# Optimization experiments

Measured on AMD Instinct MI355X. Metric: run time of the kernel, lower is better.

## Reference

```python
import jax, jax.numpy as jnp
import numpy as np

D_MODEL = 96
D_INNER = 192   # int(ssm_ratio * d_model)
D_STATE = 16
DT_RANK = 6    # ceil(96/16)
K_GROUP = 4
B, H, W = 2, 64, 64


def _selective_scan(xs, dts, A, Bs, Cs, Dskip, dt_bias):
    """Mamba selective scan.
    xs, dts: (B, K, Di, L); A: (K, Di, N); Bs, Cs: (B, K, N, L);
    Dskip, dt_bias: (K, Di). Returns y: (B, K, Di, L)."""
    delta = jax.nn.softplus(dts + dt_bias[None, :, :, None])     # (B,K,Di,L)
    u_t = jnp.moveaxis(xs, -1, 0)      # (L,B,K,Di)
    d_t = jnp.moveaxis(delta, -1, 0)   # (L,B,K,Di)
    b_t = jnp.moveaxis(Bs, -1, 0)      # (L,B,K,N)
    c_t = jnp.moveaxis(Cs, -1, 0)      # (L,B,K,N)

    def step(h, inp):
        u, dt, b, c = inp
        dA = jnp.exp(dt[..., None] * A)                          # (B,K,Di,N)
        h = h * dA + (dt * u)[..., None] * b[:, :, None, :]      # (B,K,Di,N)
        y = jnp.einsum('bkdn,bkn->bkd', h, c)
        return h, y

    h0 = jnp.zeros(xs.shape[:3] + (A.shape[-1],), xs.dtype)
    _, ys = jax.lax.scan(step, h0, (u_t, d_t, b_t, c_t))         # (L,B,K,Di)
    return jnp.moveaxis(ys, 0, -1) + Dskip[None, :, :, None] * xs


def setup_inputs() -> dict:
    key = jax.random.key(0)
    ks = jax.random.split(key, 10)
    x = jax.random.normal(ks[0], (B, H, W, D_MODEL), dtype=jnp.float32)
    in_proj_w = jax.random.normal(ks[1], (2 * D_INNER, D_MODEL), jnp.float32) * (D_MODEL ** -0.5)
    conv_w = jax.random.normal(ks[2], (D_INNER, 1, 3, 3), jnp.float32) * 0.1   # depthwise
    conv_b = jax.random.normal(ks[3], (D_INNER,), jnp.float32) * 0.01
    x_proj_weight = jax.random.normal(ks[4], (K_GROUP, DT_RANK + 2 * D_STATE, D_INNER), jnp.float32) * (D_INNER ** -0.5)
    dt_projs_weight = jax.random.uniform(ks[5], (K_GROUP, D_INNER, DT_RANK), jnp.float32,
                                         -(DT_RANK ** -0.5), DT_RANK ** -0.5)
    # bias ~ inv_softplus(dt) for dt in [0.001, 0.1]
    dt_projs_bias = jax.random.uniform(ks[6], (K_GROUP, D_INNER), jnp.float32, -6.5, -2.5)
    # S4D real init: A_log[d, n] = log(n+1)
    A_logs = jnp.log(jnp.tile(jnp.arange(1, D_STATE + 1, dtype=jnp.float32),
                              (K_GROUP * D_INNER, 1)))
    Ds = jnp.ones((K_GROUP * D_INNER,), jnp.float32)
    out_norm_w = jnp.ones((D_INNER,), jnp.float32)
    out_norm_b = jnp.zeros((D_INNER,), jnp.float32)
    out_proj_w = jax.random.normal(ks[7], (D_MODEL, D_INNER), jnp.float32) * (D_INNER ** -0.5)
    return dict(x=x, in_proj_w=in_proj_w, conv_w=conv_w, conv_b=conv_b,
                x_proj_weight=x_proj_weight, dt_projs_weight=dt_projs_weight,
                dt_projs_bias=dt_projs_bias, A_logs=A_logs, Ds=Ds,
                out_norm_w=out_norm_w, out_norm_b=out_norm_b, out_proj_w=out_proj_w)


def reference(x, in_proj_w, conv_w, conv_b, x_proj_weight, dt_projs_weight,
              dt_projs_bias, A_logs, Ds, out_norm_w, out_norm_b, out_proj_w):
    b, h, w, _ = x.shape
    xz = x @ in_proj_w.T                              # (B,H,W,2*Di)
    xp, z = jnp.split(xz, 2, axis=-1)
    xp = jnp.transpose(xp, (0, 3, 1, 2))              # (B,Di,H,W)
    xp = jax.lax.conv_general_dilated(
        xp, conv_w, (1, 1), 'SAME', feature_group_count=conv_w.shape[0],
        dimension_numbers=('NCHW', 'OIHW', 'NCHW')) + conv_b[None, :, None, None]
    xp = jax.nn.silu(xp)
    di = xp.shape[1]
    L = h * w
    # 4-way cross-scan: row-major, col-major, and their reverses
    x_hw = xp.reshape(b, di, L)
    x_wh = jnp.transpose(xp, (0, 1, 3, 2)).reshape(b, di, L)
    x_hwwh = jnp.stack([x_hw, x_wh], axis=1)          # (B,2,Di,L)
    xs = jnp.concatenate([x_hwwh, jnp.flip(x_hwwh, axis=-1)], axis=1)  # (B,4,Di,L)

    x_dbl = jnp.einsum('bkdl,kcd->bkcl', xs, x_proj_weight)
    R = dt_projs_weight.shape[-1]
    N = A_logs.shape[-1]
    dts_r = x_dbl[:, :, :R]
    Bs = x_dbl[:, :, R:R + N]                         # (B,K,N,L)
    Cs = x_dbl[:, :, R + N:]                          # (B,K,N,L)
    dts = jnp.einsum('bkrl,kdr->bkdl', dts_r, dt_projs_weight)
    A = -jnp.exp(A_logs).reshape(K_GROUP, di, N)
    Dskip = Ds.reshape(K_GROUP, di)

    out_y = _selective_scan(xs, dts, A, Bs, Cs, Dskip, dt_projs_bias)  # (B,4,Di,L)

    # un-scan: flip back the reversed dirs, un-transpose the wh dirs, sum
    inv_y = jnp.flip(out_y[:, 2:4], axis=-1)
    wh_y = jnp.transpose(out_y[:, 1].reshape(b, di, w, h), (0, 1, 3, 2)).reshape(b, di, L)
    invwh_y = jnp.transpose(inv_y[:, 1].reshape(b, di, w, h), (0, 1, 3, 2)).reshape(b, di, L)
    y = out_y[:, 0] + inv_y[:, 0] + wh_y + invwh_y    # (B,Di,L)

    y = jnp.transpose(y, (0, 2, 1))                   # (B,L,Di)
    mu = y.mean(-1, keepdims=True)
    var = ((y - mu) ** 2).mean(-1, keepdims=True)
    y = (y - mu) * jax.lax.rsqrt(var + 1e-5) * out_norm_w + out_norm_b
    y = y.reshape(b, h, w, di) + z                    # residual with gate branch (note: add, per source)
    out = y @ out_proj_w.T                            # (B,H,W,d_model)
    return jnp.transpose(out, (0, 3, 1, 2))           # (B,d_model,H,W)
```

## Files before the change

kernel.cpp:

```cpp
#include <hip/hip_runtime.h>
#include <math.h>

#define BB 2
#define HH 64
#define WW 64
#define LL 4096
#define CIN 96
#define DI 192
#define KG 4
#define NST 16
#define RNK 6
#define NCH 128
#define CHL 32

__device__ __forceinline__ int rowmap(int k, int p) {
  if (k == 0) return p;
  if (k == 1) return ((p & 63) << 6) | (p >> 6);
  if (k == 2) return (LL - 1) - p;
  int q = (LL - 1) - p;
  return ((q & 63) << 6) | (q >> 6);
}

__device__ __forceinline__ void powers(float r, float pw[NST]) {
  pw[0] = r;
  pw[1] = r * r;
  pw[2] = pw[1] * r;
  pw[3] = pw[1] * pw[1];
  pw[4] = pw[3] * r;
  pw[5] = pw[3] * pw[1];
  pw[6] = pw[3] * pw[2];
  pw[7] = pw[3] * pw[3];
  pw[8] = pw[7] * r;
  pw[9] = pw[7] * pw[1];
  pw[10] = pw[7] * pw[2];
  pw[11] = pw[7] * pw[3];
  pw[12] = pw[7] * pw[4];
  pw[13] = pw[7] * pw[5];
  pw[14] = pw[7] * pw[6];
  pw[15] = pw[7] * pw[7];
}

__device__ __forceinline__ void softplus_sig(float x, float& delta, float& r) {
  float e = __expf(fminf(x, 20.f));
  r = __builtin_amdgcn_rcpf(1.f + e);
  delta = (x > 20.f) ? x : -__logf(r);
}

__global__ __launch_bounds__(256) void k_inproj(const float* __restrict__ x,
    const float* __restrict__ w, float* __restrict__ xp_pre, float* __restrict__ z) {
  __shared__ float xt[64 * 97];
  __shared__ float wt[64 * 97];
  const int tile = blockIdx.x, og = blockIdx.y, t = threadIdx.x;
  const int tok0 = tile * 64;
  for (int idx = t; idx < 64 * 96; idx += 256) {
    int r = idx / 96, c = idx - r * 96;
    xt[r * 97 + c] = x[(tok0 + r) * 96 + c];
    wt[r * 97 + c] = w[(og * 64 + r) * 96 + c];
  }
  __syncthreads();
  const int tr = t >> 4, tc = t & 15;
  float acc[4][4];
#pragma unroll
  for (int i = 0; i < 4; ++i)
#pragma unroll
    for (int j = 0; j < 4; ++j) acc[i][j] = 0.f;
  for (int kk = 0; kk < 96; ++kk) {
    float a[4], bv[4];
#pragma unroll
    for (int i = 0; i < 4; ++i) a[i] = xt[(tr * 4 + i) * 97 + kk];
#pragma unroll
    for (int j = 0; j < 4; ++j) bv[j] = wt[(tc * 4 + j) * 97 + kk];
#pragma unroll
    for (int i = 0; i < 4; ++i)
#pragma unroll
      for (int j = 0; j < 4; ++j) acc[i][j] += a[i] * bv[j];
  }
#pragma unroll
  for (int i = 0; i < 4; ++i) {
    int tok = tok0 + tr * 4 + i;
    int b = tok >> 12, l = tok & 4095;
#pragma unroll
    for (int j = 0; j < 4; ++j) {
      int oc = og * 64 + tc * 4 + j;
      float v = acc[i][j];
      if (oc < DI) xp_pre[(b * DI + oc) * LL + l] = v;
      else         z[tok * DI + (oc - DI)] = v;
    }
  }
}

__global__ __launch_bounds__(256) void k_conv(const float* __restrict__ xp_pre,
    const float* __restrict__ cw, const float* __restrict__ cb,
    float* __restrict__ xpT, float* __restrict__ ycomb) {
  int idx = blockIdx.x * 256 + threadIdx.x;
  ycomb[idx] = 0.f;
  int l = idx & 4095;
  int bd = idx >> 12;
  int d = bd % DI, b = bd / DI;
  int h = l >> 6, wq = l & 63;
  const float* base = xp_pre + bd * LL;
  const float* wf = cw + d * 9;
  float acc = cb[d];
#pragma unroll
  for (int dh = -1; dh <= 1; ++dh) {
    int h2 = h + dh;
    if (h2 < 0 || h2 >= HH) continue;
#pragma unroll
    for (int dw = -1; dw <= 1; ++dw) {
      int w2 = wq + dw;
      if (w2 < 0 || w2 >= WW) continue;
      acc += base[h2 * WW + w2] * wf[(dh + 1) * 3 + (dw + 1)];
    }
  }
  float s = acc / (1.f + __expf(-acc));
  xpT[(b * LL + l) * DI + d] = s;
}

__global__ __launch_bounds__(256) void k_xdbl(const float* __restrict__ xpT,
    const float* __restrict__ xpw, float* __restrict__ xdT) {
  __shared__ float xs[32 * 196];
  __shared__ float wt[40 * 196];
  const int bk = blockIdx.x, tile = blockIdx.y, t = threadIdx.x;
  const int b = bk >> 2, k = bk & 3;
  for (int idx = t; idx < 32 * 192; idx += 256) {
    int r = idx / 192, c = idx - r * 192;
    xs[r * 196 + c] = xpT[(b * LL + rowmap(k, tile * 32 + r)) * DI + c];
  }
  for (int idx = t; idx < 40 * 192; idx += 256) {
    int r = idx / 192, c = idx - r * 192;
    wt[r * 196 + c] = (r < 38) ? xpw[k * 38 * 192 + idx] : 0.f;
  }
  __syncthreads();
  const int j = t >> 3;
  const int c0 = t & 7;
  float acc[5] = {0.f, 0.f, 0.f, 0.f, 0.f};
  const float4* xs4 = (const float4*)xs + j * 49;
  for (int d4 = 0; d4 < 48; ++d4) {
    float4 xv = xs4[d4];
#pragma unroll
    for (int jj = 0; jj < 5; ++jj) {
      const float4 wv = ((const float4*)wt)[(c0 + 8 * jj) * 49 + d4];
      acc[jj] += xv.x * wv.x + xv.y * wv.y + xv.z * wv.z + xv.w * wv.w;
    }
  }
  const int tok = bk * LL + tile * 32 + j;
#pragma unroll
  for (int jj = 0; jj < 5; ++jj) {
    int c = c0 + 8 * jj;
    if (c < 38) {
      int oc = (c < 6) ? 32 + c : c - 6;
      xdT[tok * 40 + oc] = acc[jj];
    }
  }
}

__global__ __launch_bounds__(192) void k_scanA(const float* __restrict__ xdT,
    const float* __restrict__ xpT, const float* __restrict__ dtw,
    const float* __restrict__ dtb, float* __restrict__ hfin, float* __restrict__ dsum) {
  const int d = threadIdx.x, bk = blockIdx.x, ch = blockIdx.y;
  const int b = bk >> 2, k = bk & 3;
  float w[RNK];
#pragma unroll
  for (int r = 0; r < RNK; ++r) w[r] = dtw[(k * DI + d) * RNK + r];
  const float bias = dtb[k * DI + d];
  float h[NST];
#pragma unroll
  for (int n = 0; n < NST; ++n) h[n] = 0.f;
  float ds = 0.f;
  const float* row = xdT + ((size_t)bk * LL + ch * CHL) * 40;
  const float* ubase = xpT + (size_t)b * LL * DI;
#pragma unroll 4
  for (int ll = 0; ll < CHL; ++ll) {
    int p = ch * CHL + ll;
    const float4* r4 = (const float4*)(row + ll * 40);
    float4 b0 = r4[0], b1 = r4[1], b2 = r4[2], b3 = r4[3];
    float4 dt4 = r4[8];
    float2 dt2 = ((const float2*)(row + ll * 40 + 36))[0];
    float xr = bias + dt4.x * w[0] + dt4.y * w[1] + dt4.z * w[2] + dt4.w * w[3]
             + dt2.x * w[4] + dt2.y * w[5];
    float delta, rdec;
    softplus_sig(xr, delta, rdec);
    float u = ubase[rowmap(k, p) * DI + d];
    float du = delta * u;
    ds += delta;
    float pw[NST];
    powers(rdec, pw);
    const float bn[NST] = {b0.x, b0.y, b0.z, b0.w, b1.x, b1.y, b1.z, b1.w,
                           b2.x, b2.y, b2.z, b2.w, b3.x, b3.y, b3.z, b3.w};
#pragma unroll
    for (int n = 0; n < NST; ++n) h[n] = h[n] * pw[n] + du * bn[n];
  }
  float4* hf = (float4*)(hfin + ((size_t)(bk * DI + d) * NCH + ch) * NST);
#pragma unroll
  for (int n = 0; n < 4; ++n)
    hf[n] = make_float4(h[4 * n], h[4 * n + 1], h[4 * n + 2], h[4 * n + 3]);
  dsum[(bk * DI + d) * NCH + ch] = ds;
}

__global__ __launch_bounds__(256) void k_scanB(const float* __restrict__ hfin,
    const float* __restrict__ dsum, const float* __restrict__ A_logs, float* __restrict__ hin) {
  int idx = blockIdx.x * 256 + threadIdx.x;
  int n = idx & 15, bkd = idx >> 4;
  int d = bkd % DI, k = (bkd / DI) & 3;
  float A = -__expf(A_logs[(k * DI + d) * NST + n]);
  float s = 0.f;
  for (int c = 0; c < NCH; ++c) {
    int o = (bkd * NCH + c) * NST + n;
    float f = hfin[o];
    hin[o] = s;
    s = s * __expf(A * dsum[bkd * NCH + c]) + f;
  }
}

__global__ __launch_bounds__(192) void k_scanC(const float* __restrict__ xdT,
    const float* __restrict__ xpT, const float* __restrict__ dtw,
    const float* __restrict__ dtb, const float* __restrict__ hin, float* __restrict__ ycomb) {
  const int d = threadIdx.x, bk = blockIdx.x, ch = blockIdx.y;
  const int b = bk >> 2, k = bk & 3;
  float w[RNK];
#pragma unroll
  for (int r = 0; r < RNK; ++r) w[r] = dtw[(k * DI + d) * RNK + r];
  const float bias = dtb[k * DI + d];
  float h[NST];
  const float4* hi = (const float4*)(hin + ((size_t)(bk * DI + d) * NCH + ch) * NST);
#pragma unroll
  for (int n = 0; n < 4; ++n) {
    float4 v = hi[n];
    h[4 * n] = v.x; h[4 * n + 1] = v.y; h[4 * n + 2] = v.z; h[4 * n + 3] = v.w;
  }
  const float* row = xdT + ((size_t)bk * LL + ch * CHL) * 40;
  const float* ubase = xpT + (size_t)b * LL * DI;
  float* yb = ycomb + (size_t)b * LL * DI;
#pragma unroll 4
  for (int ll = 0; ll < CHL; ++ll) {
    int p = ch * CHL + ll;
    const float4* r4 = (const float4*)(row + ll * 40);
    float4 b0 = r4[0], b1 = r4[1], b2 = r4[2], b3 = r4[3];
    float4 c0 = r4[4], c1 = r4[5], c2 = r4[6], c3 = r4[7];
    float4 dt4 = r4[8];
    float2 dt2 = ((const float2*)(row + ll * 40 + 36))[0];
    float xr = bias + dt4.x * w[0] + dt4.y * w[1] + dt4.z * w[2] + dt4.w * w[3]
             + dt2.x * w[4] + dt2.y * w[5];
    float delta, rdec;
    softplus_sig(xr, delta, rdec);
    int rr = rowmap(k, p);
    float u = ubase[rr * DI + d];
    float du = delta * u;
    float pw[NST];
    powers(rdec, pw);
    const float bn[NST] = {b0.x, b0.y, b0.z, b0.w, b1.x, b1.y, b1.z, b1.w,
                           b2.x, b2.y, b2.z, b2.w, b3.x, b3.y, b3.z, b3.w};
    const float cn[NST] = {c0.x, c0.y, c0.z, c0.w, c1.x, c1.y, c1.z, c1.w,
                           c2.x, c2.y, c2.z, c2.w, c3.x, c3.y, c3.z, c3.w};
    float y = 0.f;
#pragma unroll
    for (int n = 0; n < NST; ++n) {
      h[n] = h[n] * pw[n] + du * bn[n];
      y += h[n] * cn[n];
    }
    atomicAdd(&yb[rr * DI + d], y);
  }
}

__global__ __launch_bounds__(256) void k_norm(const float* __restrict__ ycomb,
    const float* __restrict__ xpT, const float* __restrict__ Ds, const float* __restrict__ z,
    const float* __restrict__ nw, const float* __restrict__ nb, float* __restrict__ yn) {
  int row = blockIdx.x * 4 + (threadIdx.x >> 6);
  int lane = threadIdx.x & 63;
  float v[3];
#pragma unroll
  for (int i = 0; i < 3; ++i) {
    int d = lane + i * 64;
    float dsv = Ds[d] + Ds[DI + d] + Ds[2 * DI + d] + Ds[3 * DI + d];
    v[i] = ycomb[row * DI + d] + dsv * xpT[row * DI + d];
  }
  float s1 = v[0] + v[1] + v[2];
  float s2 = v[0] * v[0] + v[1] * v[1] + v[2] * v[2];
#pragma unroll
  for (int off = 32; off >= 1; off >>= 1) {
    s1 += __shfl_xor(s1, off);
    s2 += __shfl_xor(s2, off);
  }
  float mu = s1 * (1.f / DI);
  float var = s2 * (1.f / DI) - mu * mu;
  float rstd = rsqrtf(var + 1e-5f);
#pragma unroll
  for (int i = 0; i < 3; ++i) {
    int d = lane + i * 64;
    yn[row * DI + d] = (v[i] - mu) * rstd * nw[d] + nb[d] + z[row * DI + d];
  }
}

__global__ __launch_bounds__(256) void k_outproj(const float* __restrict__ yn,
    const float* __restrict__ opw, float* __restrict__ out) {
  __shared__ float yt[32 * 193];
  __shared__ float wt[32 * 193];
  const int tile = blockIdx.x, og = blockIdx.y, t = threadIdx.x;
  const int tok0 = tile * 32;
  for (int idx = t; idx < 32 * 192; idx += 256) {
    int r = idx / 192, c = idx - r * 192;
    yt[r * 193 + c] = yn[(tok0 + r) * DI + c];
    wt[r * 193 + c] = opw[(og * 32 + r) * DI + c];
  }
  __syncthreads();
  const int tr = t >> 4, tc = t & 15;
  float acc[2][2] = {{0.f, 0.f}, {0.f, 0.f}};
  for (int dd = 0; dd < 192; ++dd) {
    float a0 = yt[(tr * 2) * 193 + dd], a1 = yt[(tr * 2 + 1) * 193 + dd];
    float b0 = wt[(tc * 2) * 193 + dd], b1 = wt[(tc * 2 + 1) * 193 + dd];
    acc[0][0] += a0 * b0; acc[0][1] += a0 * b1;
    acc[1][0] += a1 * b0; acc[1][1] += a1 * b1;
  }
#pragma unroll
  for (int i = 0; i < 2; ++i) {
    int tok = tok0 + tr * 2 + i;
    int b = tok >> 12, l = tok & 4095;
#pragma unroll
    for (int j = 0; j < 2; ++j) {
      int oc = og * 32 + tc * 2 + j;
      out[(b * CIN + oc) * LL + l] = acc[i][j];
    }
  }
}

extern "C" void kernel_launch(void* const* d_in, const int* in_sizes, int n_in,
                              void* d_out, int out_size, void* d_ws, size_t ws_size,
                              hipStream_t stream) {
  const float* x    = (const float*)d_in[0];
  const float* ipw  = (const float*)d_in[1];
  const float* cw   = (const float*)d_in[2];
  const float* cb   = (const float*)d_in[3];
  const float* xpw  = (const float*)d_in[4];
  const float* dtw  = (const float*)d_in[5];
  const float* dtb  = (const float*)d_in[6];
  const float* Alog = (const float*)d_in[7];
  const float* Ds   = (const float*)d_in[8];
  const float* nw   = (const float*)d_in[9];
  const float* nb   = (const float*)d_in[10];
  const float* opw  = (const float*)d_in[11];
  float* out = (float*)d_out;
  float* ws = (float*)d_ws;

  float* xp_pre = ws;
  float* xpT    = ws + 1572864;
  float* z      = ws + 3145728;
  float* xdT    = ws + 4718592;
  float* hfin   = ws + 6029312;
  float* hin    = ws + 9175040;
  float* dsum   = ws + 12320768;
  float* ycomb  = ws + 12517376;
  float* yn     = xp_pre;

  k_inproj<<<dim3(128, 6), 256, 0, stream>>>(x, ipw, xp_pre, z);
  k_conv<<<6144, 256, 0, stream>>>(xp_pre, cw, cb, xpT, ycomb);
  k_xdbl<<<dim3(8, 128), 256, 0, stream>>>(xpT, xpw, xdT);
  k_scanA<<<dim3(8, NCH), 192, 0, stream>>>(xdT, xpT, dtw, dtb, hfin, dsum);
  k_scanB<<<96, 256, 0, stream>>>(hfin, dsum, Alog, hin);
  k_scanC<<<dim3(8, NCH), 192, 0, stream>>>(xdT, xpT, dtw, dtb, hin, ycomb);
  k_norm<<<2048, 256, 0, stream>>>(ycomb, xpT, Ds, z, nw, nb, yn);
  k_outproj<<<dim3(256, 3), 256, 0, stream>>>(yn, opw, out);
}
```

Measured before the change: 230.8 us.

## Store x_dbl in spatial order, tile conv in shared memory, restructure x_proj

Result: slower. 301.4 us (+30.6%).

```diff
diff --git a/kernel.cpp b/kernel.cpp
--- a/kernel.cpp
+++ b/kernel.cpp
@@ -22,22 +22,12 @@
 }
 
 __device__ __forceinline__ void powers(float r, float pw[NST]) {
-  pw[0] = r;
-  pw[1] = r * r;
-  pw[2] = pw[1] * r;
-  pw[3] = pw[1] * pw[1];
-  pw[4] = pw[3] * r;
-  pw[5] = pw[3] * pw[1];
-  pw[6] = pw[3] * pw[2];
+  pw[0] = r;  pw[1] = r * r;  pw[2] = pw[1] * r;  pw[3] = pw[1] * pw[1];
+  pw[4] = pw[3] * r;  pw[5] = pw[3] * pw[1];  pw[6] = pw[3] * pw[2];
   pw[7] = pw[3] * pw[3];
-  pw[8] = pw[7] * r;
-  pw[9] = pw[7] * pw[1];
-  pw[10] = pw[7] * pw[2];
-  pw[11] = pw[7] * pw[3];
-  pw[12] = pw[7] * pw[4];
-  pw[13] = pw[7] * pw[5];
-  pw[14] = pw[7] * pw[6];
-  pw[15] = pw[7] * pw[7];
+  pw[8] = pw[7] * r;  pw[9] = pw[7] * pw[1];  pw[10] = pw[7] * pw[2];
+  pw[11] = pw[7] * pw[3];  pw[12] = pw[7] * pw[4];  pw[13] = pw[7] * pw[5];
+  pw[14] = pw[7] * pw[6];  pw[15] = pw[7] * pw[7];
 }
 
 __device__ __forceinline__ void softplus_sig(float x, float& delta, float& r) {
@@ -92,65 +82,92 @@
 __global__ __launch_bounds__(256) void k_conv(const float* __restrict__ xp_pre,
     const float* __restrict__ cw, const float* __restrict__ cb,
     float* __restrict__ xpT, float* __restrict__ ycomb) {
-  int idx = blockIdx.x * 256 + threadIdx.x;
-  ycomb[idx] = 0.f;
-  int l = idx & 4095;
-  int bd = idx >> 12;
-  int d = bd % DI, b = bd / DI;
-  int h = l >> 6, wq = l & 63;
-  const float* base = xp_pre + bd * LL;
-  const float* wf = cw + d * 9;
-  float acc = cb[d];
-#pragma unroll
-  for (int dh = -1; dh <= 1; ++dh) {
-    int h2 = h + dh;
-    if (h2 < 0 || h2 >= HH) continue;
-#pragma unroll
-    for (int dw = -1; dw <= 1; ++dw) {
-      int w2 = wq + dw;
-      if (w2 < 0 || w2 >= WW) continue;
-      acc += base[h2 * WW + w2] * wf[(dh + 1) * 3 + (dw + 1)];
-    }
-  }
-  float s = acc / (1.f + __expf(-acc));
-  xpT[(b * LL + l) * DI + d] = s;
+  __shared__ float ls[3 * 64 * 67];
+  const int t = threadIdx.x;
+  const int h = blockIdx.x;
+  const int b = blockIdx.y / 3, d0 = (blockIdx.y % 3) * 64;
+  int gid = (blockIdx.y * 64 + blockIdx.x) * 256 + t;
+#pragma unroll
+  for (int j = 0; j < 16; ++j) ycomb[gid + 98304 * j] = 0.f;
+  for (int i = t; i < 3 * 64; i += 256) {
+    ls[i * 67 + 0] = 0.f;
+    ls[i * 67 + 65] = 0.f;
+  }
+  for (int i = t; i < 3 * 64 * 64; i += 256) {
+    int rr = i >> 12, rem = i & 4095;
+    int dl = rem >> 6, w = rem & 63;
+    int h2 = h + rr - 1;
+    float v = (h2 >= 0 && h2 < HH)
+        ? xp_pre[((size_t)(b * DI + d0 + dl)) * LL + h2 * WW + w] : 0.f;
+    ls[(rr * 64 + dl) * 67 + w + 1] = v;
+  }
+  __syncthreads();
+  const int dl = t & 63, wg = t >> 6;
+  const int d = d0 + dl;
+  float wf[9];
+#pragma unroll
+  for (int j = 0; j < 9; ++j) wf[j] = cw[d * 9 + j];
+  const float bias = cb[d];
+#pragma unroll 4
+  for (int i = 0; i < 16; ++i) {
+    int w = wg + 4 * i;
+    float acc = bias;
+#pragma unroll
+    for (int rr = 0; rr < 3; ++rr)
+#pragma unroll
+      for (int dw = 0; dw < 3; ++dw)
+        acc += ls[(rr * 64 + dl) * 67 + w + dw] * wf[rr * 3 + dw];
+    float s = acc / (1.f + __expf(-acc));
+    xpT[((size_t)(b * LL + h * WW + w)) * DI + d] = s;
+  }
 }
 
 __global__ __launch_bounds__(256) void k_xdbl(const float* __restrict__ xpT,
     const float* __restrict__ xpw, float* __restrict__ xdT) {
-  __shared__ float xs[32 * 196];
-  __shared__ float wt[40 * 196];
-  const int bk = blockIdx.x, tile = blockIdx.y, t = threadIdx.x;
-  const int b = bk >> 2, k = bk & 3;
-  for (int idx = t; idx < 32 * 192; idx += 256) {
-    int r = idx / 192, c = idx - r * 192;
-    xs[r * 196 + c] = xpT[(b * LL + rowmap(k, tile * 32 + r)) * DI + c];
-  }
-  for (int idx = t; idx < 40 * 192; idx += 256) {
-    int r = idx / 192, c = idx - r * 192;
-    wt[r * 196 + c] = (r < 38) ? xpw[k * 38 * 192 + idx] : 0.f;
-  }
-  __syncthreads();
-  const int j = t >> 3;
-  const int c0 = t & 7;
-  float acc[5] = {0.f, 0.f, 0.f, 0.f, 0.f};
-  const float4* xs4 = (const float4*)xs + j * 49;
-  for (int d4 = 0; d4 < 48; ++d4) {
-    float4 xv = xs4[d4];
-#pragma unroll
-    for (int jj = 0; jj < 5; ++jj) {
-      const float4 wv = ((const float4*)wt)[(c0 + 8 * jj) * 49 + d4];
-      acc[jj] += xv.x * wv.x + xv.y * wv.y + xv.z * wv.z + xv.w * wv.w;
+  __shared__ float ls[64 * 193];
+  const int t = threadIdx.x;
+  const int b = blockIdx.x >> 6, tok0 = (blockIdx.x & 63) << 6;
+  const float4* src = (const float4*)(xpT + ((size_t)b * LL + tok0) * DI);
+  for (int i = t; i < 64 * 48; i += 256) {
+    int r = i / 48, c4 = i - r * 48;
+    float4 v = src[r * 48 + c4];
+    float* dst = ls + r * 193 + c4 * 4;
+    dst[0] = v.x; dst[1] = v.y; dst[2] = v.z; dst[3] = v.w;
+  }
+  __syncthreads();
+  const int lane = t & 63;
+  const int k = __builtin_amdgcn_readfirstlane(t >> 6);
+  const float* wk = xpw + k * 38 * 192;
+  float acc[38];
+#pragma unroll
+  for (int c = 0; c < 38; ++c) acc[c] = 0.f;
+  const float* xrow = ls + lane * 193;
+  for (int ch = 0; ch < 24; ++ch) {
+    float xv[8];
+#pragma unroll
+    for (int j = 0; j < 8; ++j) xv[j] = xrow[ch * 8 + j];
+#pragma unroll
+    for (int c = 0; c < 38; ++c) {
+      const float* wr = wk + c * 192 + ch * 8;
+#pragma unroll
+      for (int j = 0; j < 8; ++j) acc[c] += wr[j] * xv[j];
     }
   }
-  const int tok = bk * LL + tile * 32 + j;
-#pragma unroll
-  for (int jj = 0; jj < 5; ++jj) {
-    int c = c0 + 8 * jj;
-    if (c < 38) {
-      int oc = (c < 6) ? 32 + c : c - 6;
-      xdT[tok * 40 + oc] = acc[jj];
-    }
+  __syncthreads();
+  float* patch = ls + k * (64 * 41);
+#pragma unroll
+  for (int c = 0; c < 38; ++c) {
+    int oc = (c < 6) ? 32 + c : c - 6;
+    patch[lane * 41 + oc] = acc[c];
+  }
+  patch[lane * 41 + 38] = 0.f;
+  patch[lane * 41 + 39] = 0.f;
+  float* obase = xdT + ((size_t)(b * 4 + k) * LL + tok0) * 40;
+#pragma unroll
+  for (int i = 0; i < 40; ++i) {
+    int g = lane + 64 * i;
+    int tok = g / 40, oc = g - tok * 40;
+    obase[g] = patch[tok * 41 + oc];
   }
 }
 
@@ -167,20 +184,21 @@
 #pragma unroll
   for (int n = 0; n < NST; ++n) h[n] = 0.f;
   float ds = 0.f;
-  const float* row = xdT + ((size_t)bk * LL + ch * CHL) * 40;
+  const float* rbase = xdT + (size_t)bk * LL * 40;
   const float* ubase = xpT + (size_t)b * LL * DI;
 #pragma unroll 4
   for (int ll = 0; ll < CHL; ++ll) {
     int p = ch * CHL + ll;
-    const float4* r4 = (const float4*)(row + ll * 40);
+    int rr = rowmap(k, p);
+    const float4* r4 = (const float4*)(rbase + (size_t)rr * 40);
     float4 b0 = r4[0], b1 = r4[1], b2 = r4[2], b3 = r4[3];
     float4 dt4 = r4[8];
-    float2 dt2 = ((const float2*)(row + ll * 40 + 36))[0];
+    float2 dt2 = ((const float2*)(rbase + (size_t)rr * 40 + 36))[0];
     float xr = bias + dt4.x * w[0] + dt4.y * w[1] + dt4.z * w[2] + dt4.w * w[3]
              + dt2.x * w[4] + dt2.y * w[5];
     float delta, rdec;
     softplus_sig(xr, delta, rdec);
-    float u = ubase[rowmap(k, p) * DI + d];
+    float u = ubase[rr * DI + d];
     float du = delta * u;
     ds += delta;
     float pw[NST];
@@ -228,22 +246,22 @@
     float4 v = hi[n];
     h[4 * n] = v.x; h[4 * n + 1] = v.y; h[4 * n + 2] = v.z; h[4 * n + 3] = v.w;
   }
-  const float* row = xdT + ((size_t)bk * LL + ch * CHL) * 40;
+  const float* rbase = xdT + (size_t)bk * LL * 40;
   const float* ubase = xpT + (size_t)b * LL * DI;
   float* yb = ycomb + (size_t)b * LL * DI;
 #pragma unroll 4
   for (int ll = 0; ll < CHL; ++ll) {
     int p = ch * CHL + ll;
-    const float4* r4 = (const float4*)(row + ll * 40);
+    int rr = rowmap(k, p);
+    const float4* r4 = (const float4*)(rbase + (size_t)rr * 40);
     float4 b0 = r4[0], b1 = r4[1], b2 = r4[2], b3 = r4[3];
     float4 c0 = r4[4], c1 = r4[5], c2 = r4[6], c3 = r4[7];
     float4 dt4 = r4[8];
-    float2 dt2 = ((const float2*)(row + ll * 40 + 36))[0];
+    float2 dt2 = ((const float2*)(rbase + (size_t)rr * 40 + 36))[0];
     float xr = bias + dt4.x * w[0] + dt4.y * w[1] + dt4.z * w[2] + dt4.w * w[3]
              + dt2.x * w[4] + dt2.y * w[5];
     float delta, rdec;
     softplus_sig(xr, delta, rdec);
-    int rr = rowmap(k, p);
     float u = ubase[rr * DI + d];
     float du = delta * u;
     float pw[NST];
@@ -352,8 +370,8 @@
   float* yn     = xp_pre;
 
   k_inproj<<<dim3(128, 6), 256, 0, stream>>>(x, ipw, xp_pre, z);
-  k_conv<<<6144, 256, 0, stream>>>(xp_pre, cw, cb, xpT, ycomb);
-  k_xdbl<<<dim3(8, 128), 256, 0, stream>>>(xpT, xpw, xdT);
+  k_conv<<<dim3(64, 6), 256, 0, stream>>>(xp_pre, cw, cb, xpT, ycomb);
+  k_xdbl<<<128, 256, 0, stream>>>(xpT, xpw, xdT);
   k_scanA<<<dim3(8, NCH), 192, 0, stream>>>(xdT, xpT, dtw, dtb, hfin, dsum);
   k_scanB<<<96, 256, 0, stream>>>(hfin, dsum, Alog, hin);
   k_scanC<<<dim3(8, NCH), 192, 0, stream>>>(xdT, xpT, dtw, dtb, hin, ycomb);
```
